# Optimization experiments

Measured on AMD Instinct MI355X. Metric: run time of the kernel, lower is better.

Reference implementation:

```python
import jax, jax.numpy as jnp
import numpy as np

NUM_GROUPS = 32
EPS = 1e-6


def group_norm(x, weight, bias):
    # x: [b, c, h, w]
    b, c, h, w = x.shape
    xg = x.reshape(b, NUM_GROUPS, c // NUM_GROUPS, h, w)
    mean = jnp.mean(xg, axis=(2, 3, 4), keepdims=True)
    var = jnp.var(xg, axis=(2, 3, 4), keepdims=True)
    xn = ((xg - mean) * jax.lax.rsqrt(var + EPS)).reshape(b, c, h, w)
    return xn * weight[None, :, None, None] + bias[None, :, None, None]


def conv1x1(x, w, b):
    # 1x1 conv == per-pixel matmul. x: [b, c_in, h, w], w: [c_out, c_in]
    return jnp.einsum('oi,bihw->bohw', w, x) + b[None, :, None, None]


def setup_inputs() -> dict:
    key = jax.random.key(0)
    ks = jax.random.split(key, 9)
    b, c, h, w = 8, 512, 64, 64
    scale = 1.0 / np.sqrt(c)
    return {
        'x': jax.random.normal(ks[0], (b, c, h, w), jnp.float32),
        'gn_weight': jnp.ones((c,), jnp.float32),
        'gn_bias': jnp.zeros((c,), jnp.float32),
        'wq': jax.random.normal(ks[1], (c, c), jnp.float32) * scale,
        'bq': jnp.zeros((c,), jnp.float32),
        'wk': jax.random.normal(ks[2], (c, c), jnp.float32) * scale,
        'bk': jnp.zeros((c,), jnp.float32),
        'wv': jax.random.normal(ks[3], (c, c), jnp.float32) * scale,
        'bv': jnp.zeros((c,), jnp.float32),
        'wp': jax.random.normal(ks[4], (c, c), jnp.float32) * scale,
        'bp': jnp.zeros((c,), jnp.float32),
    }


def reference(x, gn_weight, gn_bias, wq, bq, wk, bk, wv, bv, wp, bp):
    h_ = group_norm(x, gn_weight, gn_bias)
    q = conv1x1(h_, wq, bq)
    k = conv1x1(h_, wk, bk)
    v = conv1x1(h_, wv, bv)
    b, c, h, w = q.shape
    n = h * w
    qf = q.reshape(b, c, n)
    kf = k.reshape(b, c, n)
    vf = v.reshape(b, c, n)
    # scores: [b, q, k]
    scores = jnp.einsum('bcq,bck->bqk', qf, kf) * (c ** -0.5)
    attn = jax.nn.softmax(scores, axis=-1)
    out = jnp.einsum('bqk,bck->bcq', attn, vf).reshape(b, c, h, w)
    out = conv1x1(out, wp, bp)
    return x + out
```

## Files before the change

kernel.cpp:

```cpp
#include <hip/hip_runtime.h>
#include <cstdint>

typedef unsigned short u16;
typedef __bf16 bf16x8 __attribute__((ext_vector_type(8)));
typedef float f32x4 __attribute__((ext_vector_type(4)));

__device__ __forceinline__ u16 f2bf(float f) {
    uint32_t u = __float_as_uint(f);
    u += 0x7FFFu + ((u >> 16) & 1u);
    return (u16)(u >> 16);
}
__device__ __forceinline__ float bf2f(u16 v) {
    return __uint_as_float((uint32_t)v << 16);
}

__device__ __forceinline__ void gload16(const u16* g, u16* l) {
    __builtin_amdgcn_global_load_lds(
        (const __attribute__((address_space(1))) uint32_t*)g,
        (__attribute__((address_space(3))) uint32_t*)l, 16, 0, 0);
}

__device__ __forceinline__ void swz(int& n_idx, int& m_idx, int& z_idx) {
    const int nx = gridDim.x, ny = gridDim.y;
    int lid = blockIdx.x + nx * (blockIdx.y + ny * blockIdx.z);
// ... 128 lines not shown
        int li = it * 256 + t;
        int c = li >> 3;
        int pj = (li & 7) * 8;
        float v[8];
        if (mode) {
            const float* xr = (const float*)x_raw + ((size_t)b * 512 + c) * 4096 + p0 + pj;
            float4 a = *(const float4*)xr;
            float4 d = *(const float4*)(xr + 4);
            v[0] = a.x; v[1] = a.y; v[2] = a.z; v[3] = a.w;
            v[4] = d.x; v[5] = d.y; v[6] = d.z; v[7] = d.w;
        } else {
            const u16* xr = (const u16*)x_raw + ((size_t)b * 512 + c) * 4096 + p0 + pj;
            uint4 a = *(const uint4*)xr;
            uint32_t w[4] = {a.x, a.y, a.z, a.w};
            for (int j = 0; j < 4; j++) {
                v[2 * j] = __uint_as_float(w[j] << 16);
                v[2 * j + 1] = __uint_as_float(w[j] & 0xFFFF0000u);
            }
        }
        float sc = sSc[c], sh = sSh[c];
        for (int k = 0; k < 8; k++)
            tile[(pj + k) * TPAD + c] = f2bf(v[k] * sc + sh);
    }
    __syncthreads();
    u16* H = HT + (size_t)b * 2097152 + (size_t)p0 * 512;
    for (int it = 0; it < 16; it++) {
        int ch = it * 256 + t;
        int pp = ch >> 6;
        int cc = (ch & 63) * 8;
        *(uint4*)&H[(size_t)pp * 512 + cc] = *(const uint4*)&tile[pp * TPAD + cc];
    }
}

__device__ __forceinline__ void gemm_core(const u16* __restrict__ A,
                                          const u16* __restrict__ BT,
                                          int lda, int ldb, int K,
                                          int m0, int n0,
                                          u16* lA, u16* lB,
                                          f32x4 (&acc)[4][4]) {
    const int t = threadIdx.x;
    const int wave = t >> 6, lane = t & 63;
    const int wm = (wave >> 1) * 64, wn = (wave & 1) * 64;
    const int mf = lane & 15, quad = lane >> 4;
    const int srow = t >> 3;
    const int scol = (((t & 7) ^ (srow & 7)) * 8);
    const u16* Ap = A + (size_t)(m0 + srow) * lda + scol;
    const u16* Bp = BT + (size_t)(n0 + srow) * ldb + scol;
    u16* lAd = &lA[t * 8];
    u16* lBd = &lB[t * 8];
    const int fx = mf & 7;

    for (int i = 0; i < 4; i++)
        for (int j = 0; j < 4; j++)
            acc[i][j] = (f32x4){0.f, 0.f, 0.f, 0.f};

    for (int k0 = 0; k0 < K; k0 += 64) {
        __syncthreads();
        gload16(Ap + k0, lAd);
        gload16(Ap + k0 + (size_t)32 * lda, lAd + 2048);
        gload16(Ap + k0 + (size_t)64 * lda, lAd + 4096);
        gload16(Ap + k0 + (size_t)96 * lda, lAd + 6144);
        gload16(Bp + k0, lBd);
        gload16(Bp + k0 + (size_t)32 * ldb, lBd + 2048);
        gload16(Bp + k0 + (size_t)64 * ldb, lBd + 4096);
        gload16(Bp + k0 + (size_t)96 * ldb, lBd + 6144);
        __syncthreads();
        for (int ks = 0; ks < 2; ks++) {
            bf16x8 af[4], bfr[4];
            const int sl = ((ks * 4 + quad) ^ fx) * 8;
            for (int i = 0; i < 4; i++)
                af[i] = *(const bf16x8*)&lA[(wm + i * 16 + mf) * 64 + sl];
            for (int j = 0; j < 4; j++)
                bfr[j] = *(const bf16x8*)&lB[(wn + j * 16 + mf) * 64 + sl];
            for (int i = 0; i < 4; i++)
                for (int j = 0; j < 4; j++)
                    acc[i][j] = __builtin_amdgcn_mfma_f32_16x16x32_bf16(af[i], bfr[j], acc[i][j], 0, 0, 0);
        }
    }
}

__global__ __launch_bounds__(256) void k_qkv(const u16* __restrict__ HT,
                                             const u16* __restrict__ Wc,
                                             const u16* __restrict__ Bc,
                                             u16* __restrict__ QT,
                                             u16* __restrict__ KT,
                                             u16* __restrict__ V) {
    __shared__ __align__(16) u16 sm[16384];
    int nI, mI, zI;
    swz(nI, mI, zI);
    const int b = zI / 3, s = zI % 3;
    const u16* Bb = Bc + 1024 + s * 512;
    int m0, n0, ldo, bias_by_row;
    const u16 *A, *BT;
    u16* O;
    if (s < 2) {
        m0 = mI * 128; n0 = nI * 128;
        A = HT + (size_t)b * 2097152; BT = Wc + (size_t)s * 262144;
        O = (s == 0 ? QT : KT) + (size_t)b * 2097152; ldo = 512; bias_by_row = 0;
    } else {
        m0 = nI * 128; n0 = mI * 128;
        A = Wc + (size_t)2 * 262144; BT = HT + (size_t)b * 2097152;
        O = V + (size_t)b * 2097152; ldo = 4096; bias_by_row = 1;
    }
    f32x4 acc[4][4];
    gemm_core(A, BT, 512, 512, 512, m0, n0, sm, sm + 8192, acc);

    const int t = threadIdx.x;
    const int wave = t >> 6, lane = t & 63;
    const int wm = (wave >> 1) * 64, wn = (wave & 1) * 64;
    const int mf = lane & 15, quad = lane >> 4;
    __syncthreads();
    for (int i = 0; i < 4; i++)
        for (int r = 0; r < 4; r++) {
            int row = wm + i * 16 + quad * 4 + r;
            int kk = ((row >> 2) & 3) << 4;
            for (int j = 0; j < 4; j++) {
                int col = wn + j * 16 + mf;
                float bias = bf2f(Bb[bias_by_row ? (m0 + row) : (n0 + col)]);
                sm[row * 128 + (col ^ kk)] = f2bf(acc[i][j][r] + bias);
            }
        }
    __syncthreads();
    for (int p = 0; p < 8; p++) {
        int idx = p * 256 + t;
        int rowt = idx >> 4, c8 = (idx & 15) * 8;
        int kk = ((rowt >> 2) & 3) << 4;
        uint4 v = *(const uint4*)&sm[rowt * 128 + (c8 ^ kk)];
        *(uint4*)&O[(size_t)(m0 + rowt) * ldo + n0 + c8] = v;
    }
}

__device__ __forceinline__ u16* s_ptr(u16* S_ht, u16* S_tail, int l) {
    return l == 0 ? S_ht : S_tail + (size_t)(l - 1) * 16777216;
}

__global__ __launch_bounds__(256) void k_scores(const u16* __restrict__ QT,
                                                const u16* __restrict__ KT,
                                                u16* __restrict__ S_ht,
                                                u16* __restrict__ S_tail,
                                                float* __restrict__ Part,
                                                int b0) {
    __shared__ __align__(16) u16 sm[16384];
    int nI, mI, l;
    swz(nI, mI, l);
    const int n0 = nI * 128;
    const int m0 = mI * 128;
    const int b = b0 + l;
    f32x4 acc[4][4];
    gemm_core(QT + (size_t)b * 2097152, KT + (size_t)b * 2097152, 512, 512, 512,
              m0, n0, sm, sm + 8192, acc);

    const float scale = 0.04419417382415922f;
    const int t = threadIdx.x;
    const int wave = t >> 6, lane = t & 63;
    const int wm = (wave >> 1) * 64, wn = (wave & 1) * 64;
    const int mf = lane & 15, quad = lane >> 4;
    __syncthreads();
    for (int i = 0; i < 4; i++)
        for (int r = 0; r < 4; r++) {
            int row = wm + i * 16 + quad * 4 + r;
            int kk = ((row >> 2) & 3) << 4;
            for (int j = 0; j < 4; j++) {
                int col = wn + j * 16 + mf;
                sm[row * 128 + (col ^ kk)] = f2bf(__expf(acc[i][j][r] * scale));
            }
        }
    __syncthreads();
    u16* Sb = s_ptr(S_ht, S_tail, l);
    float* pr = Part + ((size_t)b * 32 + nI) * 4096 + m0;
    for (int p = 0; p < 8; p++) {
        int idx = p * 256 + t;
        int rowt = idx >> 4, c8 = (idx & 15) * 8;
        int kk = ((rowt >> 2) & 3) << 4;
        uint4 v = *(const uint4*)&sm[rowt * 128 + (c8 ^ kk)];
        uint32_t w[4] = {v.x, v.y, v.z, v.w};
        float s = 0.f;
        for (int q2 = 0; q2 < 4; q2++)
            s += __uint_as_float(w[q2] << 16) + __uint_as_float(w[q2] & 0xFFFF0000u);
        for (int off = 8; off > 0; off >>= 1) s += __shfl_xor(s, off);
        if ((lane & 15) == 0) pr[rowt] = s;
        *(uint4*)&Sb[(size_t)(m0 + rowt) * 4096 + n0 + c8] = v;
    }
}

__global__ __launch_bounds__(256) void k_pv_split(u16* __restrict__ S_ht,
                                                  u16* __restrict__ S_tail,
                                                  const u16* __restrict__ V,
                                                  u16* __restrict__ QT,
                                                  u16* __restrict__ KT,
                                                  int b0) {
    __shared__ __align__(16) u16 sm[16384];
    int nI, mI, zI;
    swz(nI, mI, zI);
    const int n0 = nI * 128;
    const int m0 = mI * 128;
    const int l = zI >> 1, split = zI & 1, b = b0 + l;
    const u16* A = s_ptr(S_ht, S_tail, l) + split * 2048;
    const u16* BT = V + (size_t)b * 2097152 + split * 2048;
    f32x4 acc[4][4];
    gemm_core(A, BT, 4096, 4096, 2048, m0, n0, sm, sm + 8192, acc);

    const int t = threadIdx.x;
    const int wave = t >> 6, lane = t & 63;
    const int wm = (wave >> 1) * 64, wn = (wave & 1) * 64;
    const int mf = lane & 15, quad = lane >> 4;
    u16* P = (split == 0 ? QT : KT) + (size_t)b * 2097152;
    __syncthreads();
    for (int i = 0; i < 4; i++)
        for (int r = 0; r < 4; r++) {
            int row = wm + i * 16 + quad * 4 + r;
            int kk = ((row >> 2) & 3) << 4;
            for (int j = 0; j < 4; j++) {
                int col = wn + j * 16 + mf;
                sm[row * 128 + (col ^ kk)] = f2bf(acc[i][j][r]);
            }
        }
    __syncthreads();
    for (int p = 0; p < 8; p++) {
        int idx = p * 256 + t;
        int rowt = idx >> 4, c8 = (idx & 15) * 8;
        int kk = ((rowt >> 2) & 3) << 4;
        uint4 v = *(const uint4*)&sm[rowt * 128 + (c8 ^ kk)];
        *(uint4*)&P[(size_t)(m0 + rowt) * 512 + n0 + c8] = v;
    }
}

__global__ __launch_bounds__(256) void k_pv_reduce(const u16* __restrict__ QT,
                                                   const u16* __restrict__ KT,
                                                   const float* __restrict__ Part,
                                                   u16* __restrict__ OT,
                                                   int b0) {
    const int b = b0 + blockIdx.y;
    const int t = threadIdx.x;
    __shared__ float sInv[4];
    if (t < 128) {
        int r = t >> 5, which = t & 31;
        int p = blockIdx.x * 4 + r;
        float v = Part[((size_t)b * 32 + which) * 4096 + p];
        for (int off = 16; off > 0; off >>= 1) v += __shfl_xor(v, off);
        if (which == 0) sInv[r] = 1.f / v;
    }
    __syncthreads();
    const float inv = sInv[t >> 6];
    size_t base = (size_t)b * 2097152;
    size_t i0 = base + ((size_t)blockIdx.x * 256 + t) * 8;
    uint4 a = *(const uint4*)(QT + i0);
    uint4 c = *(const uint4*)(KT + i0);
    uint32_t wa[4] = {a.x, a.y, a.z, a.w};
    uint32_t wc[4] = {c.x, c.y, c.z, c.w};
    uint32_t o[4];
    for (int j = 0; j < 4; j++) {
        float lo = (__uint_as_float(wa[j] << 16) + __uint_as_float(wc[j] << 16)) * inv;
        float hi = (__uint_as_float(wa[j] & 0xFFFF0000u) + __uint_as_float(wc[j] & 0xFFFF0000u)) * inv;
        o[j] = (uint32_t)f2bf(lo) | ((uint32_t)f2bf(hi) << 16);
    }
    *(uint4*)(OT + i0) = make_uint4(o[0], o[1], o[2], o[3]);
}

__global__ __launch_bounds__(256) void k_proj(const u16* __restrict__ Wc,
                                              const u16* __restrict__ OT,
                                              const u16* __restrict__ Bc,
                                              const void* __restrict__ x_raw,
                                              const int* __restrict__ flag,
                                              void* __restrict__ y_raw) {
    __shared__ __align__(16) u16 smu[16384];
    float* smf = (float*)smu;
    int nI, mI, b;
    swz(nI, mI, b);
    const int n0 = nI * 128;
    const int m0 = mI * 128;
    f32x4 acc[4][4];
    gemm_core(Wc + (size_t)3 * 262144, OT + (size_t)b * 2097152, 512, 512, 512,
              m0, n0, smu, smu + 8192, acc);

    const int mode = *flag;
    const u16* bp = Bc + 5 * 512;
    const int t = threadIdx.x;
    const int wave = t >> 6, lane = t & 63;
    const int wn = (wave & 1) * 64;
    const int mf = lane & 15, quad = lane >> 4;
    const int whalf = wave >> 1;
    size_t bb = (size_t)b * 2097152;
    for (int h = 0; h < 2; h++) {
        __syncthreads();
        if (whalf == h) {
            for (int i = 0; i < 4; i++)
                for (int r = 0; r < 4; r++) {
                    int rowl = i * 16 + quad * 4 + r;
                    int kf = ((rowl >> 2) & 1) << 4;
                    for (int j = 0; j < 4; j++) {
                        int col = wn + j * 16 + mf;
                        smf[rowl * 128 + (col ^ kf)] = acc[i][j][r];
                    }
                }
        }
        __syncthreads();
        const int rowbase = m0 + h * 64;
        if (mode) {
            for (int p = 0; p < 8; p++) {
                int idx = p * 256 + t;
                int rowl = idx >> 5, c4 = (idx & 31) * 4;
                int kf = ((rowl >> 2) & 1) << 4;
                f32x4 v = *(const f32x4*)&smf[rowl * 128 + (c4 ^ kf)];
                int rowg = rowbase + rowl;
                float bias = bf2f(bp[rowg]);
                size_t o = bb + (size_t)rowg * 4096 + n0 + c4;
                float4 xv = *(const float4*)((const float*)x_raw + o);
                float4 out = make_float4(v[0] + bias + xv.x, v[1] + bias + xv.y,
                                         v[2] + bias + xv.z, v[3] + bias + xv.w);
                *(float4*)((float*)y_raw + o) = out;
            }
        } else {
            for (int p = 0; p < 4; p++) {
                int idx = p * 256 + t;
                int rowl = idx >> 4, c8 = (idx & 15) * 8;
                int kf = ((rowl >> 2) & 1) << 4;
                const float* sp = &smf[rowl * 128 + (c8 ^ kf)];
                f32x4 v0 = *(const f32x4*)sp;
                f32x4 v1 = *(const f32x4*)(sp + 4);
                int rowg = rowbase + rowl;
                float bias = bf2f(bp[rowg]);
                size_t o = bb + (size_t)rowg * 4096 + n0 + c8;
                uint4 xv = *(const uint4*)((const u16*)x_raw + o);
                uint32_t xw[4] = {xv.x, xv.y, xv.z, xv.w};
                float vals[8] = {v0[0], v0[1], v0[2], v0[3],
                                 v1[0], v1[1], v1[2], v1[3]};
                uint32_t ow[4];
                for (int q2 = 0; q2 < 4; q2++) {
                    float lo = __uint_as_float(xw[q2] << 16) + vals[2 * q2] + bias;
                    float hi = __uint_as_float(xw[q2] & 0xFFFF0000u) + vals[2 * q2 + 1] + bias;
                    ow[q2] = (uint32_t)f2bf(lo) | ((uint32_t)f2bf(hi) << 16);
                }
                *(uint4*)((u16*)y_raw + o) = make_uint4(ow[0], ow[1], ow[2], ow[3]);
            }
        }
    }
}

extern "C" void kernel_launch(void* const* d_in, const int* in_sizes, int n_in,
                              void* d_out, int out_size, void* d_ws, size_t ws_size,
                              hipStream_t stream) {
    (void)in_sizes; (void)n_in; (void)out_size;
    const void* x  = d_in[0];
    const void* gw = d_in[1];
    const void* gb = d_in[2];
    const void* wq = d_in[3];
    const void* bq = d_in[4];
    const void* wk = d_in[5];
    const void* bk = d_in[6];
    const void* wv = d_in[7];
    const void* bv = d_in[8];
    const void* wp = d_in[9];
    const void* bp = d_in[10];

    u16* ws16 = (u16*)d_ws;
    int* flag = (int*)d_ws;
    float* Sc = (float*)(ws16 + 16);
    float* Sh = Sc + 4096;
    u16* Wc = ws16 + 16 + 16384;
    u16* Bc = Wc + 1048576;
    u16* HT = Bc + 4096;
    u16* QT = HT + 16777216;
    u16* KT = QT + 16777216;
    u16* V  = KT + 16777216;
    u16* OT = V  + 16777216;
    float* Part = (float*)(OT + 16777216);
    u16* Tail = (u16*)(Part + 1048576);
    const size_t base_elems = (size_t)(Tail - ws16);

    int nb = 1;
    for (int cand = 8; cand >= 2; cand >>= 1) {
        size_t need = 2ull * (base_elems + (size_t)(cand - 1) * 16777216ull);
        if (ws_size >= need) { nb = cand; break; }
    }

    k_detect<<<1, 256, 0, stream>>>((const u16*)x, flag);
    k_cvt_wb<<<4108, 256, 0, stream>>>(wq, wk, wv, wp, gw, gb, bq, bk, bv, bp,
                                       flag, Wc, Bc);
    k_gn_stats<<<256, 256, 0, stream>>>(x, Bc, flag, Sc, Sh);
    k_gn_apply<<<dim3(64, 8), 256, 0, stream>>>(x, flag, Sc, Sh, HT);
    k_qkv<<<dim3(4, 32, 24), 256, 0, stream>>>(HT, Wc, Bc, QT, KT, V);
    for (int b0 = 0; b0 < 8; b0 += nb) {
        k_scores<<<dim3(32, 32, nb), 256, 0, stream>>>(QT, KT, HT, Tail, Part, b0);
        k_pv_split<<<dim3(4, 32, 2 * nb), 256, 0, stream>>>(HT, Tail, V, QT, KT, b0);
        k_pv_reduce<<<dim3(1024, nb), 256, 0, stream>>>(QT, KT, Part, OT, b0);
    }
    k_proj<<<dim3(32, 4, 8), 256, 0, stream>>>(Wc, OT, Bc, x, flag, d_out);
}
```

Baseline: 759.1 us.

## Enlarge GEMM tiles to 256x256 with 512 threads and double-buffered LDS

The shared GEMM core is templated on tile height and now uses 8 waves with 256-row or 128-row by 256-column output tiles. The qkv, scores and proj kernels move to 256x256 tiles and pv_split to 128x256. The K loop now double-buffers its LDS stages, so the next tile loads while the current one computes, and the epilogue swizzles are rewritten for the wider tiles. Scores now produces 16 partial row sums instead of 32, and the reduce kernel is updated to match. The aim is more data reuse per block and hiding global-load latency, at the cost of far more LDS per block (up to 128KB) and more accumulator registers, which lowers occupancy.

```diff
diff --git a/kernel.cpp b/kernel.cpp
--- a/kernel.cpp
+++ b/kernel.cpp
@@ -184,101 +184,126 @@
     }
 }
 
+template<int BM>
 __device__ __forceinline__ void gemm_core(const u16* __restrict__ A,
                                           const u16* __restrict__ BT,
                                           int lda, int ldb, int K,
                                           int m0, int n0,
-                                          u16* lA, u16* lB,
-                                          f32x4 (&acc)[4][4]) {
-    const int t = threadIdx.x;
-    const int wave = t >> 6, lane = t & 63;
-    const int wm = (wave >> 1) * 64, wn = (wave & 1) * 64;
+                                          u16* lds,
+                                          f32x4 (&acc)[BM / 32][4]) {
+    const int t = threadIdx.x;
+    const int lane = t & 63;
+    const int wave = t >> 6;
+    const int wm = (wave >> 2) * (BM / 2), wn = (wave & 3) * 64;
     const int mf = lane & 15, quad = lane >> 4;
     const int srow = t >> 3;
     const int scol = (((t & 7) ^ (srow & 7)) * 8);
     const u16* Ap = A + (size_t)(m0 + srow) * lda + scol;
     const u16* Bp = BT + (size_t)(n0 + srow) * ldb + scol;
-    u16* lAd = &lA[t * 8];
-    u16* lBd = &lB[t * 8];
     const int fx = mf & 7;
-
-    for (int i = 0; i < 4; i++)
+    const int ASZ = BM * 64;
+    u16* lA0 = lds;
+    u16* lA1 = lds + ASZ;
+    u16* lB0 = lds + 2 * ASZ;
+    u16* lB1 = lds + 2 * ASZ + 16384;
+
+    for (int i = 0; i < BM / 32; i++)
         for (int j = 0; j < 4; j++)
             acc[i][j] = (f32x4){0.f, 0.f, 0.f, 0.f};
 
-    for (int k0 = 0; k0 < K; k0 += 64) {
-        __syncthreads();
-        gload16(Ap + k0, lAd);
-        gload16(Ap + k0 + (size_t)32 * lda, lAd + 2048);
-        gload16(Ap + k0 + (size_t)64 * lda, lAd + 4096);
-        gload16(Ap + k0 + (size_t)96 * lda, lAd + 6144);
-        gload16(Bp + k0, lBd);
-        gload16(Bp + k0 + (size_t)32 * ldb, lBd + 2048);
-        gload16(Bp + k0 + (size_t)64 * ldb, lBd + 4096);
-        gload16(Bp + k0 + (size_t)96 * ldb, lBd + 6144);
-        __syncthreads();
+    auto stage = [&](u16* lA, u16* lB, int k0) {
+        u16* lAd = lA + t * 8;
+        u16* lBd = lB + t * 8;
+#pragma unroll
+        for (int p = 0; p < BM / 64; p++)
+            gload16(Ap + k0 + (size_t)(64 * p) * lda, lAd + p * 4096);
+#pragma unroll
+        for (int p = 0; p < 4; p++)
+            gload16(Bp + k0 + (size_t)(64 * p) * ldb, lBd + p * 4096);
+    };
+    auto compute = [&](const u16* lA, const u16* lB) {
+#pragma unroll
         for (int ks = 0; ks < 2; ks++) {
-            bf16x8 af[4], bfr[4];
+            bf16x8 af[BM / 32], bfr[4];
             const int sl = ((ks * 4 + quad) ^ fx) * 8;
-            for (int i = 0; i < 4; i++)
+#pragma unroll
+            for (int i = 0; i < BM / 32; i++)
                 af[i] = *(const bf16x8*)&lA[(wm + i * 16 + mf) * 64 + sl];
+#pragma unroll
             for (int j = 0; j < 4; j++)
                 bfr[j] = *(const bf16x8*)&lB[(wn + j * 16 + mf) * 64 + sl];
-            for (int i = 0; i < 4; i++)
+#pragma unroll
+            for (int i = 0; i < BM / 32; i++)
+#pragma unroll
                 for (int j = 0; j < 4; j++)
                     acc[i][j] = __builtin_amdgcn_mfma_f32_16x16x32_bf16(af[i], bfr[j], acc[i][j], 0, 0, 0);
         }
-    }
-}
-
-__global__ __launch_bounds__(256) void k_qkv(const u16* __restrict__ HT,
-                                             const u16* __restrict__ Wc,
-                                             const u16* __restrict__ Bc,
-                                             u16* __restrict__ QT,
-                                             u16* __restrict__ KT,
-                                             u16* __restrict__ V) {
-    __shared__ __align__(16) u16 sm[16384];
-    int nI, mI, zI;
-    swz(nI, mI, zI);
-    const int b = zI / 3, s = zI % 3;
+    };
+
+    stage(lA0, lB0, 0);
+    __syncthreads();
+    const int nt = K / 64;
+    for (int tt = 0; tt < nt; tt++) {
+        const int cur = tt & 1;
+        if (tt + 1 < nt)
+            stage(cur ? lA0 : lA1, cur ? lB0 : lB1, (tt + 1) * 64);
+        compute(cur ? lA1 : lA0, cur ? lB1 : lB0);
+        __syncthreads();
+    }
+}
+
+
+__global__ __launch_bounds__(512, 2) void k_qkv(const u16* __restrict__ HT,
+                                                const u16* __restrict__ Wc,
+                                                const u16* __restrict__ Bc,
+                                                u16* __restrict__ QT,
+                                                u16* __restrict__ KT,
+                                                u16* __restrict__ V) {
+    __shared__ __align__(16) u16 lds[65536];
+    int tI, bs, dz;
+    swz(tI, bs, dz);
+    const int b = bs / 3, s = bs % 3;
     const u16* Bb = Bc + 1024 + s * 512;
     int m0, n0, ldo, bias_by_row;
     const u16 *A, *BT;
     u16* O;
     if (s < 2) {
-        m0 = mI * 128; n0 = nI * 128;
+        m0 = (tI >> 1) * 256; n0 = (tI & 1) * 256;
         A = HT + (size_t)b * 2097152; BT = Wc + (size_t)s * 262144;
         O = (s == 0 ? QT : KT) + (size_t)b * 2097152; ldo = 512; bias_by_row = 0;
     } else {
-        m0 = nI * 128; n0 = mI * 128;
+        m0 = (tI & 1) * 256; n0 = (tI >> 1) * 256;
         A = Wc + (size_t)2 * 262144; BT = HT + (size_t)b * 2097152;
         O = V + (size_t)b * 2097152; ldo = 4096; bias_by_row = 1;
     }
-    f32x4 acc[4][4];
-    gemm_core(A, BT, 512, 512, 512, m0, n0, sm, sm + 8192, acc);
+    f32x4 acc[8][4];
+    gemm_core<256>(A, BT, 512, 512, 512, m0, n0, lds, acc);
 
     const int t = threadIdx.x;
     const int wave = t >> 6, lane = t & 63;
-    const int wm = (wave >> 1) * 64, wn = (wave & 1) * 64;
+    const int wm = (wave >> 2) * 128, wn = (wave & 3) * 64;
     const int mf = lane & 15, quad = lane >> 4;
-    __syncthreads();
-    for (int i = 0; i < 4; i++)
+#pragma unroll
+    for (int i = 0; i < 8; i++)
+#pragma unroll
         for (int r = 0; r < 4; r++) {
             int row = wm + i * 16 + quad * 4 + r;
-            int kk = ((row >> 2) & 3) << 4;
+            int key = row & 7;
+#pragma unroll
             for (int j = 0; j < 4; j++) {
                 int col = wn + j * 16 + mf;
                 float bias = bf2f(Bb[bias_by_row ? (m0 + row) : (n0 + col)]);
-                sm[row * 128 + (col ^ kk)] = f2bf(acc[i][j][r] + bias);
-            }
-        }
-    __syncthreads();
-    for (int p = 0; p < 8; p++) {
-        int idx = p * 256 + t;
-        int rowt = idx >> 4, c8 = (idx & 15) * 8;
-        int kk = ((rowt >> 2) & 3) << 4;
-        uint4 v = *(const uint4*)&sm[rowt * 128 + (c8 ^ kk)];
-        *(uint4*)&O[(size_t)(m0 + rowt) * ldo + n0 + c8] = v;
+                lds[row * 256 + (((col >> 3) ^ key) << 3) + (col & 7)] =
+                    f2bf(acc[i][j][r] + bias);
+            }
+        }
+    __syncthreads();
+#pragma unroll
+    for (int p = 0; p < 16; p++) {
+        int idx = p * 512 + t;
+        int row = idx >> 5, chunk = idx & 31;
+        uint4 v = *(const uint4*)&lds[row * 256 + ((chunk ^ (row & 7)) << 3)];
+        *(uint4*)&O[(size_t)(m0 + row) * ldo + n0 + chunk * 8] = v;
     }
 }
 
@@ -286,94 +311,100 @@
     return l == 0 ? S_ht : S_tail + (size_t)(l - 1) * 16777216;
 }
 
-__global__ __launch_bounds__(256) void k_scores(const u16* __restrict__ QT,
-                                                const u16* __restrict__ KT,
-                                                u16* __restrict__ S_ht,
-                                                u16* __restrict__ S_tail,
-                                                float* __restrict__ Part,
-                                                int b0) {
-    __shared__ __align__(16) u16 sm[16384];
+__global__ __launch_bounds__(512, 2) void k_scores(const u16* __restrict__ QT,
+                                                   const u16* __restrict__ KT,
+                                                   u16* __restrict__ S_ht,
+                                                   u16* __restrict__ S_tail,
+                                                   float* __restrict__ Part,
+                                                   int b0) {
+    __shared__ __align__(16) u16 lds[65536];
     int nI, mI, l;
     swz(nI, mI, l);
-    const int n0 = nI * 128;
-    const int m0 = mI * 128;
+    const int n0 = nI * 256;
+    const int m0 = mI * 256;
     const int b = b0 + l;
-    f32x4 acc[4][4];
-    gemm_core(QT + (size_t)b * 2097152, KT + (size_t)b * 2097152, 512, 512, 512,
-              m0, n0, sm, sm + 8192, acc);
+    f32x4 acc[8][4];
+    gemm_core<256>(QT + (size_t)b * 2097152, KT + (size_t)b * 2097152,
+                   512, 512, 512, m0, n0, lds, acc);
 
     const float scale = 0.04419417382415922f;
     const int t = threadIdx.x;
     const int wave = t >> 6, lane = t & 63;
-    const int wm = (wave >> 1) * 64, wn = (wave & 1) * 64;
+    const int wm = (wave >> 2) * 128, wn = (wave & 3) * 64;
     const int mf = lane & 15, quad = lane >> 4;
-    __syncthreads();
-    for (int i = 0; i < 4; i++)
+#pragma unroll
+    for (int i = 0; i < 8; i++)
+#pragma unroll
         for (int r = 0; r < 4; r++) {
             int row = wm + i * 16 + quad * 4 + r;
-            int kk = ((row >> 2) & 3) << 4;
+            int key = row & 7;
+#pragma unroll
             for (int j = 0; j < 4; j++) {
                 int col = wn + j * 16 + mf;
-                sm[row * 128 + (col ^ kk)] = f2bf(__expf(acc[i][j][r] * scale));
+                lds[row * 256 + (((col >> 3) ^ key) << 3) + (col & 7)] =
+                    f2bf(__expf(acc[i][j][r] * scale));
             }
         }
     __syncthreads();
     u16* Sb = s_ptr(S_ht, S_tail, l);
-    float* pr = Part + ((size_t)b * 32 + nI) * 4096 + m0;
-    for (int p = 0; p < 8; p++) {
-        int idx = p * 256 + t;
-        int rowt = idx >> 4, c8 = (idx & 15) * 8;
-        int kk = ((rowt >> 2) & 3) << 4;
-        uint4 v = *(const uint4*)&sm[rowt * 128 + (c8 ^ kk)];
+    float* pr = Part + ((size_t)b * 16 + nI) * 4096 + m0;
+#pragma unroll
+    for (int p = 0; p < 16; p++) {
+        int idx = p * 512 + t;
+        int row = idx >> 5, chunk = idx & 31;
+        uint4 v = *(const uint4*)&lds[row * 256 + ((chunk ^ (row & 7)) << 3)];
         uint32_t w[4] = {v.x, v.y, v.z, v.w};
         float s = 0.f;
         for (int q2 = 0; q2 < 4; q2++)
             s += __uint_as_float(w[q2] << 16) + __uint_as_float(w[q2] & 0xFFFF0000u);
-        for (int off = 8; off > 0; off >>= 1) s += __shfl_xor(s, off);
-        if ((lane & 15) == 0) pr[rowt] = s;
-        *(uint4*)&Sb[(size_t)(m0 + rowt) * 4096 + n0 + c8] = v;
-    }
-}
-
-__global__ __launch_bounds__(256) void k_pv_split(u16* __restrict__ S_ht,
-                                                  u16* __restrict__ S_tail,
-                                                  const u16* __restrict__ V,
-                                                  u16* __restrict__ QT,
-                                                  u16* __restrict__ KT,
-                                                  int b0) {
-    __shared__ __align__(16) u16 sm[16384];
+        for (int off = 16; off > 0; off >>= 1) s += __shfl_xor(s, off);
+        if ((lane & 31) == 0) pr[row] = s;
+        *(uint4*)&Sb[(size_t)(m0 + row) * 4096 + n0 + chunk * 8] = v;
+    }
+}
+
+__global__ __launch_bounds__(512, 2) void k_pv_split(u16* __restrict__ S_ht,
+                                                     u16* __restrict__ S_tail,
+                                                     const u16* __restrict__ V,
+                                                     u16* __restrict__ QT,
+                                                     u16* __restrict__ KT,
+                                                     int b0) {
+    __shared__ __align__(16) u16 lds[49152];
     int nI, mI, zI;
     swz(nI, mI, zI);
-    const int n0 = nI * 128;
+    const int n0 = nI * 256;
     const int m0 = mI * 128;
     const int l = zI >> 1, split = zI & 1, b = b0 + l;
     const u16* A = s_ptr(S_ht, S_tail, l) + split * 2048;
     const u16* BT = V + (size_t)b * 2097152 + split * 2048;
     f32x4 acc[4][4];
-    gemm_core(A, BT, 4096, 4096, 2048, m0, n0, sm, sm + 8192, acc);
+    gemm_core<128>(A, BT, 4096, 4096, 2048, m0, n0, lds, acc);
 
     const int t = threadIdx.x;
     const int wave = t >> 6, lane = t & 63;
-    const int wm = (wave >> 1) * 64, wn = (wave & 1) * 64;
+    const int wm = (wave >> 2) * 64, wn = (wave & 3) * 64;
     const int mf = lane & 15, quad = lane >> 4;
     u16* P = (split == 0 ? QT : KT) + (size_t)b * 2097152;
-    __syncthreads();
+#pragma unroll
     for (int i = 0; i < 4; i++)
+#pragma unroll
         for (int r = 0; r < 4; r++) {
             int row = wm + i * 16 + quad * 4 + r;
-            int kk = ((row >> 2) & 3) << 4;
+            int key = row & 7;
+#pragma unroll
             for (int j = 0; j < 4; j++) {
                 int col = wn + j * 16 + mf;
-                sm[row * 128 + (col ^ kk)] = f2bf(acc[i][j][r]);
-            }
-        }
-    __syncthreads();
+                lds[row * 256 + (((col >> 3) ^ key) << 3) + (col & 7)] =
+                    f2bf(acc[i][j][r]);
+            }
+        }
+    __syncthreads();
+#pragma unroll
     for (int p = 0; p < 8; p++) {
-        int idx = p * 256 + t;
-        int rowt = idx >> 4, c8 = (idx & 15) * 8;
-        int kk = ((rowt >> 2) & 3) << 4;
-        uint4 v = *(const uint4*)&sm[rowt * 128 + (c8 ^ kk)];
-        *(uint4*)&P[(size_t)(m0 + rowt) * 512 + n0 + c8] = v;
+        int idx = p * 512 + t;
+        int row = idx >> 5, chunk = idx & 31;
+        uint4 v = *(const uint4*)&lds[row * 256 + ((chunk ^ (row & 7)) << 3)];
+        *(uint4*)&P[(size_t)(m0 + row) * 512 + n0 + chunk * 8] = v;
     }
 }
 
@@ -385,11 +416,11 @@
     const int b = b0 + blockIdx.y;
     const int t = threadIdx.x;
     __shared__ float sInv[4];
-    if (t < 128) {
-        int r = t >> 5, which = t & 31;
+    if (t < 64) {
+        int r = t >> 4, which = t & 15;
         int p = blockIdx.x * 4 + r;
-        float v = Part[((size_t)b * 32 + which) * 4096 + p];
-        for (int off = 16; off > 0; off >>= 1) v += __shfl_xor(v, off);
+        float v = Part[((size_t)b * 16 + which) * 4096 + p];
+        for (int off = 8; off > 0; off >>= 1) v += __shfl_xor(v, off);
         if (which == 0) sInv[r] = 1.f / v;
     }
     __syncthreads();
@@ -409,70 +440,74 @@
     *(uint4*)(OT + i0) = make_uint4(o[0], o[1], o[2], o[3]);
 }
 
-__global__ __launch_bounds__(256) void k_proj(const u16* __restrict__ Wc,
-                                              const u16* __restrict__ OT,
-                                              const u16* __restrict__ Bc,
-                                              const void* __restrict__ x_raw,
-                                              const int* __restrict__ flag,
-                                              void* __restrict__ y_raw) {
-    __shared__ __align__(16) u16 smu[16384];
-    float* smf = (float*)smu;
+__global__ __launch_bounds__(512, 2) void k_proj(const u16* __restrict__ Wc,
+                                                 const u16* __restrict__ OT,
+                                                 const u16* __restrict__ Bc,
+                                                 const void* __restrict__ x_raw,
+                                                 const int* __restrict__ flag,
+                                                 void* __restrict__ y_raw) {
+    __shared__ __align__(16) u16 lds[65536];
+    float* smf = (float*)lds;
     int nI, mI, b;
     swz(nI, mI, b);
-    const int n0 = nI * 128;
-    const int m0 = mI * 128;
-    f32x4 acc[4][4];
-    gemm_core(Wc + (size_t)3 * 262144, OT + (size_t)b * 2097152, 512, 512, 512,
-              m0, n0, smu, smu + 8192, acc);
+    const int n0 = nI * 256;
+    const int m0 = mI * 256;
+    f32x4 acc[8][4];
+    gemm_core<256>(Wc + (size_t)3 * 262144, OT + (size_t)b * 2097152,
+                   512, 512, 512, m0, n0, lds, acc);
 
     const int mode = *flag;
     const u16* bp = Bc + 5 * 512;
     const int t = threadIdx.x;
     const int wave = t >> 6, lane = t & 63;
-    const int wn = (wave & 1) * 64;
+    const int wn = (wave & 3) * 64;
     const int mf = lane & 15, quad = lane >> 4;
-    const int whalf = wave >> 1;
+    const int whalf = wave >> 2;
     size_t bb = (size_t)b * 2097152;
     for (int h = 0; h < 2; h++) {
         __syncthreads();
         if (whalf == h) {
-            for (int i = 0; i < 4; i++)
+#pragma unroll
+            for (int i = 0; i < 8; i++)
+#pragma unroll
                 for (int r = 0; r < 4; r++) {
-                    int rowl = i * 16 + quad * 4 + r;
-                    int kf = ((rowl >> 2) & 1) << 4;
+                    int rl = i * 16 + quad * 4 + r;
+                    int key = rl & 7;
+#pragma unroll
                     for (int j = 0; j < 4; j++) {
                         int col = wn + j * 16 + mf;
-                        smf[rowl * 128 + (col ^ kf)] = acc[i][j][r];
+                        smf[rl * 256 + (((col >> 2) ^ key) << 2) + (col & 3)] =
+                            acc[i][j][r];
                     }
                 }
         }
         __syncthreads();
-        const int rowbase = m0 + h * 64;
+        const int rowbase = m0 + h * 128;
         if (mode) {
-            for (int p = 0; p < 8; p++) {
-                int idx = p * 256 + t;
-                int rowl = idx >> 5, c4 = (idx & 31) * 4;
-                int kf = ((rowl >> 2) & 1) << 4;
-                f32x4 v = *(const f32x4*)&smf[rowl * 128 + (c4 ^ kf)];
-                int rowg = rowbase + rowl;
+#pragma unroll
+            for (int p = 0; p < 16; p++) {
+                int idx = p * 512 + t;
+                int rl = idx >> 6, chunk = idx & 63;
+                f32x4 v = *(const f32x4*)&smf[rl * 256 + ((chunk ^ (rl & 7)) << 2)];
+                int rowg = rowbase + rl;
                 float bias = bf2f(bp[rowg]);
-                size_t o = bb + (size_t)rowg * 4096 + n0 + c4;
+                size_t o = bb + (size_t)rowg * 4096 + n0 + chunk * 4;
                 float4 xv = *(const float4*)((const float*)x_raw + o);
                 float4 out = make_float4(v[0] + bias + xv.x, v[1] + bias + xv.y,
                                          v[2] + bias + xv.z, v[3] + bias + xv.w);
                 *(float4*)((float*)y_raw + o) = out;
             }
         } else {
-            for (int p = 0; p < 4; p++) {
-                int idx = p * 256 + t;
-                int rowl = idx >> 4, c8 = (idx & 15) * 8;
-                int kf = ((rowl >> 2) & 1) << 4;
-                const float* sp = &smf[rowl * 128 + (c8 ^ kf)];
-                f32x4 v0 = *(const f32x4*)sp;
-                f32x4 v1 = *(const f32x4*)(sp + 4);
-                int rowg = rowbase + rowl;
+#pragma unroll
+            for (int p = 0; p < 8; p++) {
+                int idx = p * 512 + t;
+                int rl = idx >> 5, cp = idx & 31;
+                int c0 = (2 * cp) ^ (rl & 7), c1 = (2 * cp + 1) ^ (rl & 7);
+                f32x4 v0 = *(const f32x4*)&smf[rl * 256 + (c0 << 2)];
+                f32x4 v1 = *(const f32x4*)&smf[rl * 256 + (c1 << 2)];
+                int rowg = rowbase + rl;
                 float bias = bf2f(bp[rowg]);
-                size_t o = bb + (size_t)rowg * 4096 + n0 + c8;
+                size_t o = bb + (size_t)rowg * 4096 + n0 + cp * 8;
                 uint4 xv = *(const uint4*)((const u16*)x_raw + o);
                 uint32_t xw[4] = {xv.x, xv.y, xv.z, xv.w};
                 float vals[8] = {v0[0], v0[1], v0[2], v0[3],
@@ -531,11 +566,11 @@
                                        flag, Wc, Bc);
     k_gn_stats<<<256, 256, 0, stream>>>(x, Bc, flag, Sc, Sh);
     k_gn_apply<<<dim3(64, 8), 256, 0, stream>>>(x, flag, Sc, Sh, HT);
-    k_qkv<<<dim3(4, 32, 24), 256, 0, stream>>>(HT, Wc, Bc, QT, KT, V);
+    k_qkv<<<dim3(32, 24), 512, 0, stream>>>(HT, Wc, Bc, QT, KT, V);
     for (int b0 = 0; b0 < 8; b0 += nb) {
-        k_scores<<<dim3(32, 32, nb), 256, 0, stream>>>(QT, KT, HT, Tail, Part, b0);
-        k_pv_split<<<dim3(4, 32, 2 * nb), 256, 0, stream>>>(HT, Tail, V, QT, KT, b0);
+        k_scores<<<dim3(16, 16, nb), 512, 0, stream>>>(QT, KT, HT, Tail, Part, b0);
+        k_pv_split<<<dim3(2, 32, 2 * nb), 512, 0, stream>>>(HT, Tail, V, QT, KT, b0);
         k_pv_reduce<<<dim3(1024, nb), 256, 0, stream>>>(QT, KT, Part, OT, b0);
     }
-    k_proj<<<dim3(32, 4, 8), 256, 0, stream>>>(Wc, OT, Bc, x, flag, d_out);
-}
+    k_proj<<<dim3(16, 2, 8), 512, 0, stream>>>(Wc, OT, Bc, x, flag, d_out);
+}
```

Result: slower. 776.7 us (+2.3%).

## Double-buffer LDS tiles in shared GEMM core to overlap loads with MFMA

Applied to the files above, without the earlier changes.

Restructures the shared GEMM mainloop to use two LDS buffers for A and B, issuing the next K-tile's global-to-LDS loads before computing on the current tile. Partial vmcnt waits and raw s_barrier plus sched_barrier replace the two __syncthreads per iteration, so memory latency can be hidden behind MFMA work. LDS per block doubles to 64 KB, which may lower occupancy in every GEMM kernel. The waitcnt counting depends on exact load ordering.

```diff
diff --git a/kernel.cpp b/kernel.cpp
--- a/kernel.cpp
+++ b/kernel.cpp
@@ -188,7 +188,7 @@
                                           const u16* __restrict__ BT,
                                           int lda, int ldb, int K,
                                           int m0, int n0,
-                                          u16* lA, u16* lB,
+                                          u16* lds,
                                           f32x4 (&acc)[4][4]) {
     const int t = threadIdx.x;
     const int wave = t >> 6, lane = t & 63;
@@ -198,16 +198,19 @@
     const int scol = (((t & 7) ^ (srow & 7)) * 8);
     const u16* Ap = A + (size_t)(m0 + srow) * lda + scol;
     const u16* Bp = BT + (size_t)(n0 + srow) * ldb + scol;
-    u16* lAd = &lA[t * 8];
-    u16* lBd = &lB[t * 8];
     const int fx = mf & 7;
+    u16* lA0 = lds;
+    u16* lA1 = lds + 8192;
+    u16* lB0 = lds + 16384;
+    u16* lB1 = lds + 24576;
 
     for (int i = 0; i < 4; i++)
         for (int j = 0; j < 4; j++)
             acc[i][j] = (f32x4){0.f, 0.f, 0.f, 0.f};
 
-    for (int k0 = 0; k0 < K; k0 += 64) {
-        __syncthreads();
+    auto stage = [&](u16* la, u16* lb, int k0) {
+        u16* lAd = la + t * 8;
+        u16* lBd = lb + t * 8;
         gload16(Ap + k0, lAd);
         gload16(Ap + k0 + (size_t)32 * lda, lAd + 2048);
         gload16(Ap + k0 + (size_t)64 * lda, lAd + 4096);
@@ -216,18 +219,41 @@
         gload16(Bp + k0 + (size_t)32 * ldb, lBd + 2048);
         gload16(Bp + k0 + (size_t)64 * ldb, lBd + 4096);
         gload16(Bp + k0 + (size_t)96 * ldb, lBd + 6144);
-        __syncthreads();
+    };
+    auto compute = [&](const u16* la, const u16* lb) {
+#pragma unroll
         for (int ks = 0; ks < 2; ks++) {
             bf16x8 af[4], bfr[4];
             const int sl = ((ks * 4 + quad) ^ fx) * 8;
+#pragma unroll
             for (int i = 0; i < 4; i++)
-                af[i] = *(const bf16x8*)&lA[(wm + i * 16 + mf) * 64 + sl];
+                af[i] = *(const bf16x8*)&la[(wm + i * 16 + mf) * 64 + sl];
+#pragma unroll
             for (int j = 0; j < 4; j++)
-                bfr[j] = *(const bf16x8*)&lB[(wn + j * 16 + mf) * 64 + sl];
+                bfr[j] = *(const bf16x8*)&lb[(wn + j * 16 + mf) * 64 + sl];
+#pragma unroll
             for (int i = 0; i < 4; i++)
+#pragma unroll
                 for (int j = 0; j < 4; j++)
                     acc[i][j] = __builtin_amdgcn_mfma_f32_16x16x32_bf16(af[i], bfr[j], acc[i][j], 0, 0, 0);
         }
+    };
+
+    stage(lA0, lB0, 0);
+    const int nt = K / 64;
+    for (int tt = 0; tt < nt; tt++) {
+        const int cur = tt & 1;
+        if (tt + 1 < nt) {
+            stage(cur ? lA0 : lA1, cur ? lB0 : lB1, (tt + 1) * 64);
+            asm volatile("s_waitcnt vmcnt(8)" ::: "memory");
+        } else {
+            asm volatile("s_waitcnt vmcnt(0)" ::: "memory");
+        }
+        __builtin_amdgcn_s_barrier();
+        __builtin_amdgcn_sched_barrier(0);
+        compute(cur ? lA1 : lA0, cur ? lB1 : lB0);
+        __builtin_amdgcn_sched_barrier(0);
+        __builtin_amdgcn_s_barrier();
     }
 }
 
@@ -237,7 +263,7 @@
                                              u16* __restrict__ QT,
                                              u16* __restrict__ KT,
                                              u16* __restrict__ V) {
-    __shared__ __align__(16) u16 sm[16384];
+    __shared__ __align__(16) u16 lds[32768];
     int nI, mI, zI;
     swz(nI, mI, zI);
     const int b = zI / 3, s = zI % 3;
@@ -255,7 +281,7 @@
         O = V + (size_t)b * 2097152; ldo = 4096; bias_by_row = 1;
     }
     f32x4 acc[4][4];
-    gemm_core(A, BT, 512, 512, 512, m0, n0, sm, sm + 8192, acc);
+    gemm_core(A, BT, 512, 512, 512, m0, n0, lds, acc);
 
     const int t = threadIdx.x;
     const int wave = t >> 6, lane = t & 63;
@@ -269,7 +295,7 @@
             for (int j = 0; j < 4; j++) {
                 int col = wn + j * 16 + mf;
                 float bias = bf2f(Bb[bias_by_row ? (m0 + row) : (n0 + col)]);
-                sm[row * 128 + (col ^ kk)] = f2bf(acc[i][j][r] + bias);
+                lds[row * 128 + (col ^ kk)] = f2bf(acc[i][j][r] + bias);
             }
         }
     __syncthreads();
@@ -277,7 +303,7 @@
         int idx = p * 256 + t;
         int rowt = idx >> 4, c8 = (idx & 15) * 8;
         int kk = ((rowt >> 2) & 3) << 4;
-        uint4 v = *(const uint4*)&sm[rowt * 128 + (c8 ^ kk)];
+        uint4 v = *(const uint4*)&lds[rowt * 128 + (c8 ^ kk)];
         *(uint4*)&O[(size_t)(m0 + rowt) * ldo + n0 + c8] = v;
     }
 }
@@ -292,7 +318,7 @@
                                                 u16* __restrict__ S_tail,
                                                 float* __restrict__ Part,
                                                 int b0) {
-    __shared__ __align__(16) u16 sm[16384];
+    __shared__ __align__(16) u16 lds[32768];
     int nI, mI, l;
     swz(nI, mI, l);
     const int n0 = nI * 128;
@@ -300,7 +326,7 @@
     const int b = b0 + l;
     f32x4 acc[4][4];
     gemm_core(QT + (size_t)b * 2097152, KT + (size_t)b * 2097152, 512, 512, 512,
-              m0, n0, sm, sm + 8192, acc);
+              m0, n0, lds, acc);
 
     const float scale = 0.04419417382415922f;
     const int t = threadIdx.x;
@@ -314,7 +340,7 @@
             int kk = ((row >> 2) & 3) << 4;
             for (int j = 0; j < 4; j++) {
                 int col = wn + j * 16 + mf;
-                sm[row * 128 + (col ^ kk)] = f2bf(__expf(acc[i][j][r] * scale));
+                lds[row * 128 + (col ^ kk)] = f2bf(__expf(acc[i][j][r] * scale));
             }
         }
     __syncthreads();
@@ -324,7 +350,7 @@
         int idx = p * 256 + t;
         int rowt = idx >> 4, c8 = (idx & 15) * 8;
         int kk = ((rowt >> 2) & 3) << 4;
-        uint4 v = *(const uint4*)&sm[rowt * 128 + (c8 ^ kk)];
+        uint4 v = *(const uint4*)&lds[rowt * 128 + (c8 ^ kk)];
         uint32_t w[4] = {v.x, v.y, v.z, v.w};
         float s = 0.f;
         for (int q2 = 0; q2 < 4; q2++)
@@ -341,7 +367,7 @@
                                                   u16* __restrict__ QT,
                                                   u16* __restrict__ KT,
                                                   int b0) {
-    __shared__ __align__(16) u16 sm[16384];
+    __shared__ __align__(16) u16 lds[32768];
     int nI, mI, zI;
     swz(nI, mI, zI);
     const int n0 = nI * 128;
@@ -350,7 +376,7 @@
     const u16* A = s_ptr(S_ht, S_tail, l) + split * 2048;
     const u16* BT = V + (size_t)b * 2097152 + split * 2048;
     f32x4 acc[4][4];
-    gemm_core(A, BT, 4096, 4096, 2048, m0, n0, sm, sm + 8192, acc);
+    gemm_core(A, BT, 4096, 4096, 2048, m0, n0, lds, acc);
 
     const int t = threadIdx.x;
     const int wave = t >> 6, lane = t & 63;
@@ -364,7 +390,7 @@
             int kk = ((row >> 2) & 3) << 4;
             for (int j = 0; j < 4; j++) {
                 int col = wn + j * 16 + mf;
-                sm[row * 128 + (col ^ kk)] = f2bf(acc[i][j][r]);
+                lds[row * 128 + (col ^ kk)] = f2bf(acc[i][j][r]);
             }
         }
     __syncthreads();
@@ -372,7 +398,7 @@
         int idx = p * 256 + t;
         int rowt = idx >> 4, c8 = (idx & 15) * 8;
         int kk = ((rowt >> 2) & 3) << 4;
-        uint4 v = *(const uint4*)&sm[rowt * 128 + (c8 ^ kk)];
+        uint4 v = *(const uint4*)&lds[rowt * 128 + (c8 ^ kk)];
         *(uint4*)&P[(size_t)(m0 + rowt) * 512 + n0 + c8] = v;
     }
 }
@@ -415,15 +441,15 @@
                                               const void* __restrict__ x_raw,
                                               const int* __restrict__ flag,
                                               void* __restrict__ y_raw) {
-    __shared__ __align__(16) u16 smu[16384];
-    float* smf = (float*)smu;
+    __shared__ __align__(16) u16 lds[32768];
+    float* smf = (float*)lds;
     int nI, mI, b;
     swz(nI, mI, b);
     const int n0 = nI * 128;
     const int m0 = mI * 128;
     f32x4 acc[4][4];
     gemm_core(Wc + (size_t)3 * 262144, OT + (size_t)b * 2097152, 512, 512, 512,
-              m0, n0, smu, smu + 8192, acc);
+              m0, n0, lds, acc);
 
     const int mode = *flag;
     const u16* bp = Bc + 5 * 512;
```

Result: no change. 749.2 us (-1.3%).

## Use 256x128 output tiles for QKV, scores and projection GEMMs

Applied to the files above, without the earlier changes.

Adds a gemm256 core in which each wave computes a 128x64 sub-tile (8x4 MFMA accumulators), so each block covers a 256x128 output tile. The QKV, scores and projection kernels move to it with halved grids, and their epilogues are staged through LDS in two or four passes. The aim is more arithmetic per LDS and global load, cutting operand traffic per FLOP. In exchange it doubles accumulator registers and uses 48KB of LDS per block, which can lower occupancy, and the smaller grids may fill fewer CUs.

```diff
diff --git a/kernel.cpp b/kernel.cpp
--- a/kernel.cpp
+++ b/kernel.cpp
@@ -184,12 +184,12 @@
     }
 }
 
-__device__ __forceinline__ void gemm_core(const u16* __restrict__ A,
-                                          const u16* __restrict__ BT,
-                                          int lda, int ldb, int K,
-                                          int m0, int n0,
-                                          u16* lA, u16* lB,
-                                          f32x4 (&acc)[4][4]) {
+__device__ __forceinline__ void gemm128(const u16* __restrict__ A,
+                                        const u16* __restrict__ BT,
+                                        int lda, int ldb, int K,
+                                        int m0, int n0,
+                                        u16* lA, u16* lB,
+                                        f32x4 (&acc)[4][4]) {
     const int t = threadIdx.x;
     const int wave = t >> 6, lane = t & 63;
     const int wm = (wave >> 1) * 64, wn = (wave & 1) * 64;
@@ -231,54 +231,116 @@
     }
 }
 
-__global__ __launch_bounds__(256) void k_qkv(const u16* __restrict__ HT,
-                                             const u16* __restrict__ Wc,
-                                             const u16* __restrict__ Bc,
-                                             u16* __restrict__ QT,
-                                             u16* __restrict__ KT,
-                                             u16* __restrict__ V) {
-    __shared__ __align__(16) u16 sm[16384];
-    int nI, mI, zI;
-    swz(nI, mI, zI);
-    const int b = zI / 3, s = zI % 3;
+__device__ __forceinline__ void gemm256(const u16* __restrict__ A,
+                                        const u16* __restrict__ BT,
+                                        int lda, int ldb, int K,
+                                        int m0, int n0,
+                                        u16* lds,
+                                        f32x4 (&acc)[8][4]) {
+    const int t = threadIdx.x;
+    const int wave = t >> 6, lane = t & 63;
+    const int wm = (wave >> 1) * 128, wn = (wave & 1) * 64;
+    const int mf = lane & 15, quad = lane >> 4;
+    const int srow = t >> 3;
+    const int scol = (((t & 7) ^ (srow & 7)) * 8);
+    const u16* Ap = A + (size_t)(m0 + srow) * lda + scol;
+    const u16* Bp = BT + (size_t)(n0 + srow) * ldb + scol;
+    const int fx = mf & 7;
+    u16* lA = lds;
+    u16* lB = lds + 16384;
+    u16* lAd = lA + t * 8;
+    u16* lBd = lB + t * 8;
+
+#pragma unroll
+    for (int i = 0; i < 8; i++)
+#pragma unroll
+        for (int j = 0; j < 4; j++)
+            acc[i][j] = (f32x4){0.f, 0.f, 0.f, 0.f};
+
+    for (int k0 = 0; k0 < K; k0 += 64) {
+        __syncthreads();
+#pragma unroll
+        for (int p = 0; p < 8; p++)
+            gload16(Ap + k0 + (size_t)(32 * p) * lda, lAd + p * 2048);
+#pragma unroll
+        for (int p = 0; p < 4; p++)
+            gload16(Bp + k0 + (size_t)(32 * p) * ldb, lBd + p * 2048);
+        __syncthreads();
+#pragma unroll
+        for (int ks = 0; ks < 2; ks++) {
+            bf16x8 af[8], bfr[4];
+            const int sl = ((ks * 4 + quad) ^ fx) * 8;
+#pragma unroll
+            for (int i = 0; i < 8; i++)
+                af[i] = *(const bf16x8*)&lA[(wm + i * 16 + mf) * 64 + sl];
+#pragma unroll
+            for (int j = 0; j < 4; j++)
+                bfr[j] = *(const bf16x8*)&lB[(wn + j * 16 + mf) * 64 + sl];
+#pragma unroll
+            for (int i = 0; i < 8; i++)
+#pragma unroll
+                for (int j = 0; j < 4; j++)
+                    acc[i][j] = __builtin_amdgcn_mfma_f32_16x16x32_bf16(af[i], bfr[j], acc[i][j], 0, 0, 0);
+        }
+    }
+}
+
+__global__ __launch_bounds__(256, 2) void k_qkv(const u16* __restrict__ HT,
+                                                const u16* __restrict__ Wc,
+                                                const u16* __restrict__ Bc,
+                                                u16* __restrict__ QT,
+                                                u16* __restrict__ KT,
+                                                u16* __restrict__ V) {
+    __shared__ __align__(16) u16 lds[24576];
+    int tI, bs, z;
+    swz(tI, bs, z);
+    const int b = bs / 3, s = bs % 3;
     const u16* Bb = Bc + 1024 + s * 512;
     int m0, n0, ldo, bias_by_row;
     const u16 *A, *BT;
     u16* O;
     if (s < 2) {
-        m0 = mI * 128; n0 = nI * 128;
+        m0 = (tI >> 2) * 256; n0 = (tI & 3) * 128;
         A = HT + (size_t)b * 2097152; BT = Wc + (size_t)s * 262144;
         O = (s == 0 ? QT : KT) + (size_t)b * 2097152; ldo = 512; bias_by_row = 0;
     } else {
-        m0 = nI * 128; n0 = mI * 128;
+        m0 = (tI & 1) * 256; n0 = (tI >> 1) * 128;
         A = Wc + (size_t)2 * 262144; BT = HT + (size_t)b * 2097152;
         O = V + (size_t)b * 2097152; ldo = 4096; bias_by_row = 1;
     }
-    f32x4 acc[4][4];
-    gemm_core(A, BT, 512, 512, 512, m0, n0, sm, sm + 8192, acc);
+    f32x4 acc[8][4];
+    gemm256(A, BT, 512, 512, 512, m0, n0, lds, acc);
 
     const int t = threadIdx.x;
     const int wave = t >> 6, lane = t & 63;
-    const int wm = (wave >> 1) * 64, wn = (wave & 1) * 64;
+    const int wg = wave >> 1, wn = (wave & 1) * 64;
     const int mf = lane & 15, quad = lane >> 4;
-    __syncthreads();
-    for (int i = 0; i < 4; i++)
-        for (int r = 0; r < 4; r++) {
-            int row = wm + i * 16 + quad * 4 + r;
-            int kk = ((row >> 2) & 3) << 4;
-            for (int j = 0; j < 4; j++) {
-                int col = wn + j * 16 + mf;
-                float bias = bf2f(Bb[bias_by_row ? (m0 + row) : (n0 + col)]);
-                sm[row * 128 + (col ^ kk)] = f2bf(acc[i][j][r] + bias);
-            }
-        }
-    __syncthreads();
-    for (int p = 0; p < 8; p++) {
-        int idx = p * 256 + t;
-        int rowt = idx >> 4, c8 = (idx & 15) * 8;
-        int kk = ((rowt >> 2) & 3) << 4;
-        uint4 v = *(const uint4*)&sm[rowt * 128 + (c8 ^ kk)];
-        *(uint4*)&O[(size_t)(m0 + rowt) * ldo + n0 + c8] = v;
+    for (int h = 0; h < 2; h++) {
+        __syncthreads();
+        if (wg == h) {
+#pragma unroll
+            for (int i = 0; i < 8; i++)
+#pragma unroll
+                for (int r = 0; r < 4; r++) {
+                    int rowl = i * 16 + quad * 4 + r;
+                    int kk = ((rowl >> 2) & 3) << 4;
+#pragma unroll
+                    for (int j = 0; j < 4; j++) {
+                        int col = wn + j * 16 + mf;
+                        float bias = bf2f(Bb[bias_by_row ? (m0 + h * 128 + rowl)
+                                                        : (n0 + col)]);
+                        lds[rowl * 128 + (col ^ kk)] = f2bf(acc[i][j][r] + bias);
+                    }
+                }
+        }
+        __syncthreads();
+        for (int p = 0; p < 8; p++) {
+            int idx = p * 256 + t;
+            int rowt = idx >> 4, c8 = (idx & 15) * 8;
+            int kk = ((rowt >> 2) & 3) << 4;
+            uint4 v = *(const uint4*)&lds[rowt * 128 + (c8 ^ kk)];
+            *(uint4*)&O[(size_t)(m0 + h * 128 + rowt) * ldo + n0 + c8] = v;
+        }
     }
 }
 
@@ -286,52 +348,59 @@
     return l == 0 ? S_ht : S_tail + (size_t)(l - 1) * 16777216;
 }
 
-__global__ __launch_bounds__(256) void k_scores(const u16* __restrict__ QT,
-                                                const u16* __restrict__ KT,
-                                                u16* __restrict__ S_ht,
-                                                u16* __restrict__ S_tail,
-                                                float* __restrict__ Part,
-                                                int b0) {
-    __shared__ __align__(16) u16 sm[16384];
+__global__ __launch_bounds__(256, 2) void k_scores(const u16* __restrict__ QT,
+                                                   const u16* __restrict__ KT,
+                                                   u16* __restrict__ S_ht,
+                                                   u16* __restrict__ S_tail,
+                                                   float* __restrict__ Part,
+                                                   int b0) {
+    __shared__ __align__(16) u16 lds[24576];
     int nI, mI, l;
     swz(nI, mI, l);
     const int n0 = nI * 128;
-    const int m0 = mI * 128;
+    const int m0 = mI * 256;
     const int b = b0 + l;
-    f32x4 acc[4][4];
-    gemm_core(QT + (size_t)b * 2097152, KT + (size_t)b * 2097152, 512, 512, 512,
-              m0, n0, sm, sm + 8192, acc);
+    f32x4 acc[8][4];
+    gemm256(QT + (size_t)b * 2097152, KT + (size_t)b * 2097152, 512, 512, 512,
+            m0, n0, lds, acc);
 
     const float scale = 0.04419417382415922f;
     const int t = threadIdx.x;
     const int wave = t >> 6, lane = t & 63;
-    const int wm = (wave >> 1) * 64, wn = (wave & 1) * 64;
+    const int wg = wave >> 1, wn = (wave & 1) * 64;
     const int mf = lane & 15, quad = lane >> 4;
-    __syncthreads();
-    for (int i = 0; i < 4; i++)
-        for (int r = 0; r < 4; r++) {
-            int row = wm + i * 16 + quad * 4 + r;
-            int kk = ((row >> 2) & 3) << 4;
-            for (int j = 0; j < 4; j++) {
-                int col = wn + j * 16 + mf;
-                sm[row * 128 + (col ^ kk)] = f2bf(__expf(acc[i][j][r] * scale));
-            }
-        }
-    __syncthreads();
     u16* Sb = s_ptr(S_ht, S_tail, l);
-    float* pr = Part + ((size_t)b * 32 + nI) * 4096 + m0;
-    for (int p = 0; p < 8; p++) {
-        int idx = p * 256 + t;
-        int rowt = idx >> 4, c8 = (idx & 15) * 8;
-        int kk = ((rowt >> 2) & 3) << 4;
-        uint4 v = *(const uint4*)&sm[rowt * 128 + (c8 ^ kk)];
-        uint32_t w[4] = {v.x, v.y, v.z, v.w};
-        float s = 0.f;
-        for (int q2 = 0; q2 < 4; q2++)
-            s += __uint_as_float(w[q2] << 16) + __uint_as_float(w[q2] & 0xFFFF0000u);
-        for (int off = 8; off > 0; off >>= 1) s += __shfl_xor(s, off);
-        if ((lane & 15) == 0) pr[rowt] = s;
-        *(uint4*)&Sb[(size_t)(m0 + rowt) * 4096 + n0 + c8] = v;
+    float* pr = Part + ((size_t)b * 32 + nI) * 4096;
+    for (int h = 0; h < 2; h++) {
+        __syncthreads();
+        if (wg == h) {
+#pragma unroll
+            for (int i = 0; i < 8; i++)
+#pragma unroll
+                for (int r = 0; r < 4; r++) {
+                    int rowl = i * 16 + quad * 4 + r;
+                    int kk = ((rowl >> 2) & 3) << 4;
+#pragma unroll
+                    for (int j = 0; j < 4; j++) {
+                        int col = wn + j * 16 + mf;
+                        lds[rowl * 128 + (col ^ kk)] = f2bf(__expf(acc[i][j][r] * scale));
+                    }
+                }
+        }
+        __syncthreads();
+        for (int p = 0; p < 8; p++) {
+            int idx = p * 256 + t;
+            int rowt = idx >> 4, c8 = (idx & 15) * 8;
+            int kk = ((rowt >> 2) & 3) << 4;
+            uint4 v = *(const uint4*)&lds[rowt * 128 + (c8 ^ kk)];
+            uint32_t w[4] = {v.x, v.y, v.z, v.w};
+            float s = 0.f;
+            for (int q2 = 0; q2 < 4; q2++)
+                s += __uint_as_float(w[q2] << 16) + __uint_as_float(w[q2] & 0xFFFF0000u);
+            for (int off = 8; off > 0; off >>= 1) s += __shfl_xor(s, off);
+            if ((lane & 15) == 0) pr[m0 + h * 128 + rowt] = s;
+            *(uint4*)&Sb[(size_t)(m0 + h * 128 + rowt) * 4096 + n0 + c8] = v;
+        }
     }
 }
 
@@ -350,7 +419,7 @@
     const u16* A = s_ptr(S_ht, S_tail, l) + split * 2048;
     const u16* BT = V + (size_t)b * 2097152 + split * 2048;
     f32x4 acc[4][4];
-    gemm_core(A, BT, 4096, 4096, 2048, m0, n0, sm, sm + 8192, acc);
+    gemm128(A, BT, 4096, 4096, 2048, m0, n0, sm, sm + 8192, acc);
 
     const int t = threadIdx.x;
     const int wave = t >> 6, lane = t & 63;
@@ -409,45 +478,48 @@
     *(uint4*)(OT + i0) = make_uint4(o[0], o[1], o[2], o[3]);
 }
 
-__global__ __launch_bounds__(256) void k_proj(const u16* __restrict__ Wc,
-                                              const u16* __restrict__ OT,
-                                              const u16* __restrict__ Bc,
-                                              const void* __restrict__ x_raw,
-                                              const int* __restrict__ flag,
-                                              void* __restrict__ y_raw) {
-    __shared__ __align__(16) u16 smu[16384];
-    float* smf = (float*)smu;
+__global__ __launch_bounds__(256, 2) void k_proj(const u16* __restrict__ Wc,
+                                                 const u16* __restrict__ OT,
+                                                 const u16* __restrict__ Bc,
+                                                 const void* __restrict__ x_raw,
+                                                 const int* __restrict__ flag,
+                                                 void* __restrict__ y_raw) {
+    __shared__ __align__(16) u16 lds[24576];
+    float* smf = (float*)lds;
     int nI, mI, b;
     swz(nI, mI, b);
     const int n0 = nI * 128;
-    const int m0 = mI * 128;
-    f32x4 acc[4][4];
-    gemm_core(Wc + (size_t)3 * 262144, OT + (size_t)b * 2097152, 512, 512, 512,
-              m0, n0, smu, smu + 8192, acc);
+    const int m0 = mI * 256;
+    f32x4 acc[8][4];
+    gemm256(Wc + (size_t)3 * 262144, OT + (size_t)b * 2097152, 512, 512, 512,
+            m0, n0, lds, acc);
 
     const int mode = *flag;
     const u16* bp = Bc + 5 * 512;
     const int t = threadIdx.x;
     const int wave = t >> 6, lane = t & 63;
-    const int wn = (wave & 1) * 64;
+    const int wg = wave >> 1, wn = (wave & 1) * 64;
     const int mf = lane & 15, quad = lane >> 4;
-    const int whalf = wave >> 1;
     size_t bb = (size_t)b * 2097152;
-    for (int h = 0; h < 2; h++) {
-        __syncthreads();
-        if (whalf == h) {
-            for (int i = 0; i < 4; i++)
+    for (int q = 0; q < 4; q++) {
+        __syncthreads();
+        if (wg == (q >> 1)) {
+            const int io = (q & 1) * 4;
+#pragma unroll
+            for (int i2 = 0; i2 < 4; i2++)
+#pragma unroll
                 for (int r = 0; r < 4; r++) {
-                    int rowl = i * 16 + quad * 4 + r;
+                    int rowl = i2 * 16 + quad * 4 + r;
                     int kf = ((rowl >> 2) & 1) << 4;
+#pragma unroll
                     for (int j = 0; j < 4; j++) {
                         int col = wn + j * 16 + mf;
-                        smf[rowl * 128 + (col ^ kf)] = acc[i][j][r];
+                        smf[rowl * 128 + (col ^ kf)] = acc[io + i2][j][r];
                     }
                 }
         }
         __syncthreads();
-        const int rowbase = m0 + h * 64;
+        const int rowbase = m0 + q * 64;
         if (mode) {
             for (int p = 0; p < 8; p++) {
                 int idx = p * 256 + t;
@@ -531,11 +603,11 @@
                                        flag, Wc, Bc);
     k_gn_stats<<<256, 256, 0, stream>>>(x, Bc, flag, Sc, Sh);
     k_gn_apply<<<dim3(64, 8), 256, 0, stream>>>(x, flag, Sc, Sh, HT);
-    k_qkv<<<dim3(4, 32, 24), 256, 0, stream>>>(HT, Wc, Bc, QT, KT, V);
+    k_qkv<<<dim3(64, 24), 256, 0, stream>>>(HT, Wc, Bc, QT, KT, V);
     for (int b0 = 0; b0 < 8; b0 += nb) {
-        k_scores<<<dim3(32, 32, nb), 256, 0, stream>>>(QT, KT, HT, Tail, Part, b0);
+        k_scores<<<dim3(32, 16, nb), 256, 0, stream>>>(QT, KT, HT, Tail, Part, b0);
         k_pv_split<<<dim3(4, 32, 2 * nb), 256, 0, stream>>>(HT, Tail, V, QT, KT, b0);
         k_pv_reduce<<<dim3(1024, nb), 256, 0, stream>>>(QT, KT, Part, OT, b0);
     }
-    k_proj<<<dim3(32, 4, 8), 256, 0, stream>>>(Wc, OT, Bc, x, flag, d_out);
-}
+    k_proj<<<dim3(32, 2, 8), 256, 0, stream>>>(Wc, OT, Bc, x, flag, d_out);
+}
```

After: 1.194 ms. +57.3%, slower.
